# Kernel optimization log

Hardware: AMD Instinct MI355X
Metric: run time of the kernel (lower is better)

Reference implementation:

```python
import jax, jax.numpy as jnp
import numpy as np
import math

N = 10000; E = 160000; B = 16
H = 256; TD = 128; NB = 4; NL = 3; NAT = 100; CD = 3


def _silu(x):
    return x * jax.nn.sigmoid(x)


def _mlp2(x, w1, b1, w2, b2):
    return _silu(x @ w1 + b1) @ w2 + b2


def _ln(x, g, b):
    m = jnp.mean(x, -1, keepdims=True)
    v = jnp.mean((x - m) ** 2, -1, keepdims=True)
    return (x - m) / jnp.sqrt(v + 1e-5) * g + b


def _fwd(x_atoms, pos, edge_index, batch_idx, timesteps, conditions, emb,
         te_w1, te_b1, te_w2, te_b2, ce_w1, ce_b1, ce_w2, ce_b2,
         tp_w1, tp_b1, tp_w2, tp_b2, nm_w1, nm_b1, nm_w2, nm_b2,
         em_w1, em_b1, em_w2, em_b2, ln_g, ln_b,
         ao_w1, ao_b1, ao_w2, ao_b2, co_w1, co_b1, co_w2, co_b2):
    n = x_atoms.shape[0]
    row, col = edge_index[0], edge_index[1]  # row = source (x_j), col = target (x_i)
    h = emb[x_atoms]  # [N, H]
    half = TD // 2
    freqs = jnp.exp(jnp.arange(half, dtype=jnp.float32) * (-math.log(10000.0) / (half - 1)))
    ang = timesteps.astype(jnp.float32)[:, None] * freqs[None, :]
    time_emb = _mlp2(jnp.concatenate([jnp.sin(ang), jnp.cos(ang)], -1), te_w1, te_b1, te_w2, te_b2)
    time_emb = time_emb + _mlp2(conditions, ce_w1, ce_b1, ce_w2, ce_b2)  # [B, TD]
    rel = pos[row] - pos[col]
    dist = jnp.sqrt(jnp.sum(rel * rel, -1, keepdims=True))  # [E, 1]
    counts = jnp.maximum(
        jax.ops.segment_sum(jnp.ones((row.shape[0],), jnp.float32), col, num_segments=n), 1.0)[:, None]
    for b in range(NB):
        h = h + _mlp2(time_emb, tp_w1[b], tp_b1[b], tp_w2[b], tp_b2[b])[batch_idx]
        for l in range(NL):
            # message: edge_mlp(concat(x_i, x_j, dist)); PyG x_i = target = col, x_j = source = row
            msg = _mlp2(jnp.concatenate([h[col], h[row], dist], -1),
                        em_w1[b, l], em_b1[b, l], em_w2[b, l], em_b2[b, l])  # [E, H]
            agg = jax.ops.segment_sum(msg, col, num_segments=n) / counts  # mean aggregation
            h_new = _mlp2(h, nm_w1[b, l], nm_b1[b, l], nm_w2[b, l], nm_b2[b, l]) + agg
            h = _ln(h + h_new, ln_g[b, l], ln_b[b, l])
    atom = _mlp2(h, ao_w1, ao_b1, ao_w2, ao_b2)  # [N, NAT]
    coord = _mlp2(h, co_w1, co_b1, co_w2, co_b2)  # [N, 3]
    return atom, coord


def setup_inputs() -> dict:
    key = jax.random.key(0)
    ks = jax.random.split(key, 48)
    ki = iter(ks)

    def nrm(shape, s=0.02):
        return jax.random.normal(next(ki), shape, jnp.float32) * s

    x_atoms = jax.random.randint(next(ki), (N,), 0, NAT)
    pos = jax.random.normal(next(ki), (N, 3), jnp.float32)
    row = jax.random.randint(next(ki), (E,), 0, N)
    off = jax.random.randint(next(ki), (E,), 1, N)
    col = (row + off) % N  # avoid self-loops so dist > 0
    edge_index = jnp.stack([row, col])
    batch_idx = jnp.sort(jax.random.randint(next(ki), (N,), 0, B))
    timesteps = jax.random.randint(next(ki), (B,), 0, 1000)
    conditions = jax.random.normal(next(ki), (B, CD), jnp.float32)
    z = lambda s: jnp.zeros(s, jnp.float32)
    params = dict(
        emb=nrm((NAT, H)),
        te_w1=nrm((TD, 2 * TD)), te_b1=z((2 * TD,)), te_w2=nrm((2 * TD, TD)), te_b2=z((TD,)),
        ce_w1=nrm((CD, H)), ce_b1=z((H,)), ce_w2=nrm((H, TD)), ce_b2=z((TD,)),
        tp_w1=nrm((NB, TD, H)), tp_b1=z((NB, H)), tp_w2=nrm((NB, H, H)), tp_b2=z((NB, H)),
        nm_w1=nrm((NB, NL, H, H)), nm_b1=z((NB, NL, H)), nm_w2=nrm((NB, NL, H, H)), nm_b2=z((NB, NL, H)),
        em_w1=nrm((NB, NL, 2 * H + 1, H)), em_b1=z((NB, NL, H)), em_w2=nrm((NB, NL, H, H)), em_b2=z((NB, NL, H)),
        ln_g=jnp.ones((NB, NL, H), jnp.float32), ln_b=z((NB, NL, H)),
        ao_w1=nrm((H, H)), ao_b1=z((H,)), ao_w2=nrm((H, NAT)), ao_b2=z((NAT,)),
        co_w1=nrm((H, H)), co_b1=z((H,)), co_w2=nrm((H, 3)), co_b2=z((3,)),
    )
    return dict(x_atoms=x_atoms, pos=pos, edge_index=edge_index, batch_idx=batch_idx,
                timesteps=timesteps, conditions=conditions, **params)


def reference(x_atoms, pos, edge_index, batch_idx, timesteps, conditions, emb,
              te_w1, te_b1, te_w2, te_b2, ce_w1, ce_b1, ce_w2, ce_b2,
              tp_w1, tp_b1, tp_w2, tp_b2, nm_w1, nm_b1, nm_w2, nm_b2,
              em_w1, em_b1, em_w2, em_b2, ln_g, ln_b,
              ao_w1, ao_b1, ao_w2, ao_b2, co_w1, co_b1, co_w2, co_b2):
    return _fwd(x_atoms, pos, edge_index, batch_idx, timesteps, conditions, emb,
                te_w1, te_b1, te_w2, te_b2, ce_w1, ce_b1, ce_w2, ce_b2,
                tp_w1, tp_b1, tp_w2, tp_b2, nm_w1, nm_b1, nm_w2, nm_b2,
                em_w1, em_b1, em_w2, em_b2, ln_g, ln_b,
                ao_w1, ao_b1, ao_w2, ao_b2, co_w1, co_b1, co_w2, co_b2)
```

## Files before the change

### kernel.cpp

```cpp
#include <hip/hip_runtime.h>

typedef unsigned short u16;
typedef __attribute__((ext_vector_type(8))) short   bf16x8;
typedef __attribute__((ext_vector_type(4))) float   f32x4;
typedef __attribute__((ext_vector_type(4))) unsigned short u16x4;
typedef __attribute__((ext_vector_type(2))) unsigned short u16x2;

#define DEV __device__ __forceinline__

DEV float bf2f(u16 u){ return __uint_as_float(((unsigned)u)<<16); }
DEV u16 f2bf(float f){ unsigned x=__float_as_uint(f); unsigned r=x+0x7fffu+((x>>16)&1u); return (u16)(r>>16); }
DEV float silu_f(float x){
  float e = __expf(-x);
  return x * __builtin_amdgcn_rcpf(1.f + e);
}
DEV float ldf(const void* p, long i, int isbf){
  float r;
  if (isbf) r = bf2f(((const u16*)p)[i]);
  else      r = ((const float*)p)[i];
  return r;
}
template<int ISBF> DEV float LD(const void* p, long i){
  if (ISBF) return bf2f(((const u16*)p)[i]);
  return ((const float*)p)[i];
}

#define GLDS(g,l) __builtin_amdgcn_global_load_lds((const __attribute__((address_space(1))) void*)(g), (__attribute__((address_space(3))) void*)(l), 16, 0, 0)

__global__ void k_detect(const unsigned* __restrict__ lng, int* __restrict__ flag){
  if (threadIdx.x == 0 && blockIdx.x == 0)
    flag[0] = (lng[0] == 0x3F800000u) ? 0 : 1;
}

__global__ __launch_bounds__(256) void k_packparams(
    const void* nm_b1, const void* em_b1, const void* nm_b2, const void* em_b2,
    const void* ln_g, const void* ln_b, const void* em_w1,
    const void* ao_b1, const void* co_b1, const void* ao_b2,
    const void* co_w2, const void* co_b2,
    const int* __restrict__ flagp, float* __restrict__ pp){
  int isbf = flagp[0];
  int i = blockIdx.x*256 + threadIdx.x;
  if (i >= 22887) return;
  const int T1 = 3072;
  float v;
  if      (i < T1)    v = ldf(nm_b1, i, isbf);
  else if (i < 2*T1)  v = ldf(em_b1, i-T1, isbf);
  else if (i < 3*T1)  v = ldf(nm_b2, i-2*T1, isbf);
  else if (i < 4*T1)  v = ldf(em_b2, i-3*T1, isbf);
  else if (i < 5*T1)  v = ldf(ln_g, i-4*T1, isbf);
  else if (i < 6*T1)  v = ldf(ln_b, i-5*T1, isbf);
  else if (i < 7*T1){ int j=i-6*T1; int li=j>>8; v = ldf(em_w1, (long)li*513*256 + 512*256 + (j&255), isbf); }
  else if (i < 22016){ int j=i-21504; v = (j<256) ? ldf(ao_b1,j,isbf) : ldf(co_b1,j-256,isbf); }
  else if (i < 22116) v = ldf(ao_b2, i-22016, isbf);
  else if (i < 22884) v = ldf(co_w2, i-22116, isbf);
  else                v = ldf(co_b2, i-22884, isbf);
  pp[i] = v;
}

template<int ISBF>
DEV void wtpose_body(const void* in, long inoff, long ims, int istride, int Ncin,
                     u16* out, long obase, int ors, long oms){
  __shared__ float tile[64][65];
  int k0 = blockIdx.x*64, j0 = blockIdx.y*64;
  long m = blockIdx.z;
  int t = threadIdx.x;
  int c = t & 63, r4 = t >> 6;
  #pragma unroll
  for (int pass=0; pass<16; pass++){
    int k = k0 + pass*4 + r4;
    int j = j0 + c;
    float v = 0.f;
    if (j < Ncin) v = LD<ISBF>(in, inoff + m*ims + (long)k*istride + j);
    tile[pass*4 + r4][c] = v;
  }
  __syncthreads();
  #pragma unroll
  for (int pass=0; pass<16; pass++){
    int j = j0 + pass*4 + r4;
    int k = k0 + c;
    out[m*oms + obase + (long)j*ors + k] = f2bf(tile[c][pass*4 + r4]);
  }
}
__global__ __launch_bounds__(256) void k_wtpose(const void* in, long inoff, long ims, int istride, int Ncin,
                        u16* out, long obase, int ors, long oms, const int* __restrict__ flagp){
  if (flagp[0]) wtpose_body<1>(in, inoff, ims, istride, Ncin, out, obase, ors, oms);
  else          wtpose_body<0>(in, inoff, ims, istride, Ncin, out, obase, ors, oms);
}

template<int ISBF>
DEV void timeembed_body(const int* tsteps, const void* cond,
    const void* te_w1, const void* te_b1, const void* te_w2, const void* te_b2,
    const void* ce_w1, const void* ce_b1, const void* ce_w2, const void* ce_b2,
    float* time_emb){
  __shared__ float sa[256], sb[256];
  int b = blockIdx.x, t = threadIdx.x;
  float ts = (float)tsteps[b];
  if (t < 64){
    float coef = (float)(-9.210340371976184/63.0);
    float fr = __expf(coef * (float)t);
    float ang = ts * fr;
    sa[t]      = sinf(ang);
    sa[64 + t] = cosf(ang);
  }
  __syncthreads();
  {
    float a = LD<ISBF>(te_b1, t);
    float s0=0.f,s1=0.f,s2=0.f,s3=0.f;
    #pragma unroll
    for (int k=0;k<128;k+=4){
      s0 += sa[k  ]*LD<ISBF>(te_w1,(k  )*256+t);
      s1 += sa[k+1]*LD<ISBF>(te_w1,(k+1)*256+t);
      s2 += sa[k+2]*LD<ISBF>(te_w1,(k+2)*256+t);
      s3 += sa[k+3]*LD<ISBF>(te_w1,(k+3)*256+t);
    }
    sb[t] = silu_f(a + ((s0+s1)+(s2+s3)));
  }
  __syncthreads();
  float te = 0.f;
  if (t < 128){
    float s0=0.f,s1=0.f,s2=0.f,s3=0.f;
    #pragma unroll
    for (int k=0;k<256;k+=4){
      s0 += sb[k  ]*LD<ISBF>(te_w2,(k  )*128+t);
      s1 += sb[k+1]*LD<ISBF>(te_w2,(k+1)*128+t);
      s2 += sb[k+2]*LD<ISBF>(te_w2,(k+2)*128+t);
      s3 += sb[k+3]*LD<ISBF>(te_w2,(k+3)*128+t);
    }
    te = LD<ISBF>(te_b2, t) + ((s0+s1)+(s2+s3));
  }
  {
    float a = LD<ISBF>(ce_b1, t);
    #pragma unroll
    for (int k=0;k<3;k++) a += LD<ISBF>(cond, b*3 + k)*LD<ISBF>(ce_w1, k*256 + t);
    float v = silu_f(a);
    __syncthreads();
    sa[t] = v;
  }
  __syncthreads();
  if (t < 128){
    float s0=0.f,s1=0.f,s2=0.f,s3=0.f;
    #pragma unroll
    for (int k=0;k<256;k+=4){
      s0 += sa[k  ]*LD<ISBF>(ce_w2,(k  )*128+t);
      s1 += sa[k+1]*LD<ISBF>(ce_w2,(k+1)*128+t);
      s2 += sa[k+2]*LD<ISBF>(ce_w2,(k+2)*128+t);
      s3 += sa[k+3]*LD<ISBF>(ce_w2,(k+3)*128+t);
    }
    float ce = LD<ISBF>(ce_b2, t) + ((s0+s1)+(s2+s3));
    time_emb[b*128 + t] = te + ce;
  }
}
__global__ __launch_bounds__(256) void k_timeembed(
    const int* tsteps, const void* cond,
    const void* te_w1, const void* te_b1, const void* te_w2, const void* te_b2,
    const void* ce_w1, const void* ce_b1, const void* ce_w2, const void* ce_b2,
    const int* __restrict__ flagp, float* time_emb){
  if (flagp[0]) timeembed_body<1>(tsteps,cond,te_w1,te_b1,te_w2,te_b2,ce_w1,ce_b1,ce_w2,ce_b2,time_emb);
  else          timeembed_body<0>(tsteps,cond,te_w1,te_b1,te_w2,te_b2,ce_w1,ce_b1,ce_w2,ce_b2,time_emb);
}

template<int ISBF>
DEV void timeproj_body(const float* time_emb, const void* tp_w1, const void* tp_b1,
                       const void* tp_w2, const void* tp_b2, float* tpe){
  __shared__ float x[128];
  __shared__ float tm[256];
  int b4 = blockIdx.x >> 4, b = blockIdx.x & 15, t = threadIdx.x;
  if (t < 128) x[t] = time_emb[b*128 + t];
  __syncthreads();
  {
    float s0=0.f,s1=0.f,s2=0.f,s3=0.f;
    #pragma unroll
    for (int k=0;k<128;k+=4){
      s0 += x[k  ]*LD<ISBF>(tp_w1, ((long)b4*128 + k  )*256 + t);
      s1 += x[k+1]*LD<ISBF>(tp_w1, ((long)b4*128 + k+1)*256 + t);
      s2 += x[k+2]*LD<ISBF>(tp_w1, ((long)b4*128 + k+2)*256 + t);
      s3 += x[k+3]*LD<ISBF>(tp_w1, ((long)b4*128 + k+3)*256 + t);
    }
    float a = LD<ISBF>(tp_b1, b4*256 + t) + ((s0+s1)+(s2+s3));
    tm[t] = silu_f(a);
  }
  __syncthreads();
  float s0=0.f,s1=0.f,s2=0.f,s3=0.f;
  #pragma unroll
  for (int k=0;k<256;k+=4){
    s0 += tm[k  ]*LD<ISBF>(tp_w2, ((long)b4*256 + k  )*256 + t);
    s1 += tm[k+1]*LD<ISBF>(tp_w2, ((long)b4*256 + k+1)*256 + t);
    s2 += tm[k+2]*LD<ISBF>(tp_w2, ((long)b4*256 + k+2)*256 + t);
    s3 += tm[k+3]*LD<ISBF>(tp_w2, ((long)b4*256 + k+3)*256 + t);
  }
  float o = LD<ISBF>(tp_b2, b4*256 + t) + ((s0+s1)+(s2+s3));
  tpe[((long)b4*16 + b)*256 + t] = o;
}
__global__ __launch_bounds__(256) void k_timeproj(
    const float* time_emb, const void* tp_w1, const void* tp_b1,
    const void* tp_w2, const void* tp_b2, const int* __restrict__ flagp, float* tpe){
  if (flagp[0]) timeproj_body<1>(time_emb, tp_w1, tp_b1, tp_w2, tp_b2, tpe);
  else          timeproj_body<0>(time_emb, tp_w1, tp_b1, tp_w2, tp_b2, tpe);
}

template<int ISBF>
DEV void edgegeo_body(const int* ei, const void* pos, float* dist, int* cnt, int E){
  int e = blockIdx.x*256 + threadIdx.x;
  if (e >= E) return;
  int r = ei[e], c = ei[E + e];
  float dx = LD<ISBF>(pos,(long)r*3+0) - LD<ISBF>(pos,(long)c*3+0);
  float dy = LD<ISBF>(pos,(long)r*3+1) - LD<ISBF>(pos,(long)c*3+1);
  float dz = LD<ISBF>(pos,(long)r*3+2) - LD<ISBF>(pos,(long)c*3+2);
  dist[e] = sqrtf(dx*dx + dy*dy + dz*dz);
  atomicAdd(&cnt[c], 1);
}
__global__ __launch_bounds__(256) void k_edgegeo(const int* ei, const void* pos,
                          const int* __restrict__ flagp, float* dist, int* cnt, int E){
  if (flagp[0]) edgegeo_body<1>(ei,pos,dist,cnt,E);
  else          edgegeo_body<0>(ei,pos,dist,cnt,E);
}

__global__ __launch_bounds__(1024) void k_scan(const int* __restrict__ cnt, int* __restrict__ basep, int n){
  __shared__ int s[1024];
  int t = threadIdx.x;
  int running = 0;
  int nch = (n + 1023) >> 10;
  for (int ch=0; ch<nch; ch++){
    int i = ch*1024 + t;
    int v = (i < n) ? cnt[i] : 0;
    s[t] = v;
    __syncthreads();
    for (int off=1; off<1024; off<<=1){
      int add = (t >= off) ? s[t-off] : 0;
      __syncthreads();
      s[t] += add;
      __syncthreads();
    }
    if (i < n) basep[i] = running + s[t] - v;
    running += s[1023];
    __syncthreads();
  }
  if (t == 0) basep[n] = running;
}

__global__ __launch_bounds__(256) void k_scatter(const int* __restrict__ ei, const int* __restrict__ basep,
                          int* __restrict__ cursor, int* __restrict__ perm, int E){
  int e = blockIdx.x*256 + threadIdx.x;
  if (e >= E) return;
  int c = ei[E + e];
  int p = atomicAdd(&cursor[c], 1);
  perm[basep[c] + p] = e;
}

template<int ISBF>
DEV void embed_body(const int* xa, const void* emb, const float* tpe0, const int* bidx,
                    float* h, u16* hb, int total){
  int idx = blockIdx.x*256 + threadIdx.x;
  if (idx >= total) return;
  int row = idx >> 8, col = idx & 255;
  float v = LD<ISBF>(emb, (long)xa[row]*256 + col) + tpe0[bidx[row]*256 + col];
  h[idx] = v;
  hb[idx] = f2bf(v);
}
__global__ __launch_bounds__(256) void k_embed(const int* xa, const void* emb,
                        const int* __restrict__ flagp, const float* tpe0, const int* bidx,
                        float* h, u16* hb, int total){
  if (flagp[0]) embed_body<1>(xa, emb, tpe0, bidx, h, hb, total);
  else          embed_body<0>(xa, emb, tpe0, bidx, h, hb, total);
}

__global__ __launch_bounds__(256) void k_agg(
    const u16* __restrict__ PQ, const int* __restrict__ perm, const int* __restrict__ basep,
    const int* __restrict__ rows, const float* __restrict__ dist,
    const float* __restrict__ w1rf, const float* __restrict__ b1f,
    const int* __restrict__ cnt, u16* __restrict__ A2, int n){
  int w = threadIdx.x >> 6, lane = threadIdx.x & 63;
  int node = blockIdx.x*2 + (w >> 1);
  if (node >= n) return;
  int half = w & 1;
  int c0 = half*128 + lane*2;
  u16x2 pv = *(const u16x2*)&PQ[(long)node*512 + c0];
  float pb0 = bf2f(pv[0]) + b1f[c0];
  float pb1 = bf2f(pv[1]) + b1f[c0+1];
  float wr0 = w1rf[c0], wr1 = w1rf[c0+1];
  float acc0 = 0.f, acc1 = 0.f;
  int s = basep[node], e = basep[node+1];
  const u16* Qb = PQ + 256 + c0;
  for (int q0=s; q0<e; q0+=64){
    int m = e - q0; if (m > 64) m = 64;
    int   rl = 0; float dl = 0.f;
    if (lane < m){ int ed = perm[q0+lane]; rl = rows[ed]; dl = dist[ed]; }
    int q = 0;
    for (; q+4<=m; q+=4){
      int   r0 = __shfl(rl, q,   64), r1 = __shfl(rl, q+1, 64);
      int   r2 = __shfl(rl, q+2, 64), r3 = __shfl(rl, q+3, 64);
      float d0 = __shfl(dl, q,   64), d1 = __shfl(dl, q+1, 64);
      float d2 = __shfl(dl, q+2, 64), d3 = __shfl(dl, q+3, 64);
      u16x2 qv0 = *(const u16x2*)&Qb[(long)r0*512];
      u16x2 qv1 = *(const u16x2*)&Qb[(long)r1*512];
      u16x2 qv2 = *(const u16x2*)&Qb[(long)r2*512];
      u16x2 qv3 = *(const u16x2*)&Qb[(long)r3*512];
      acc0 += silu_f(fmaf(d0, wr0, pb0 + bf2f(qv0[0])));
      acc1 += silu_f(fmaf(d0, wr1, pb1 + bf2f(qv0[1])));
      acc0 += silu_f(fmaf(d1, wr0, pb0 + bf2f(qv1[0])));
      acc1 += silu_f(fmaf(d1, wr1, pb1 + bf2f(qv1[1])));
      acc0 += silu_f(fmaf(d2, wr0, pb0 + bf2f(qv2[0])));
      acc1 += silu_f(fmaf(d2, wr1, pb1 + bf2f(qv2[1])));
      acc0 += silu_f(fmaf(d3, wr0, pb0 + bf2f(qv3[0])));
      acc1 += silu_f(fmaf(d3, wr1, pb1 + bf2f(qv3[1])));
    }
    for (; q<m; q++){
      int   r = __shfl(rl, q, 64);
      float d = __shfl(dl, q, 64);
      u16x2 qv = *(const u16x2*)&Qb[(long)r*512];
      acc0 += silu_f(fmaf(d, wr0, pb0 + bf2f(qv[0])));
      acc1 += silu_f(fmaf(d, wr1, pb1 + bf2f(qv[1])));
    }
  }
  int cc = cnt[node];
  float inv = __builtin_amdgcn_rcpf((float)(cc > 0 ? cc : 1));
  u16x2 o; o[0] = f2bf(acc0*inv); o[1] = f2bf(acc1*inv);
  *(u16x2*)&A2[(long)node*512 + 256 + c0] = o;
}

__global__ __launch_bounds__(256) void k_co2(
    const u16* __restrict__ UV, const float* __restrict__ w, const float* __restrict__ b,
    const int* __restrict__ flagp, void* __restrict__ out, long n100, int n){
  int isbf = flagp[0];
  int row = blockIdx.x*4 + (threadIdx.x >> 6);
  if (row >= n) return;
  int lane = threadIdx.x & 63;
  int k0 = lane*4;
  u16x4 vv = *(const u16x4*)&UV[(long)row*512 + 256 + k0];
  float a0=0.f, a1=0.f, a2=0.f;
  #pragma unroll
  for (int j=0;j<4;j++){
    float v = bf2f(vv[j]);
    a0 += v*w[(k0+j)*3+0];
    a1 += v*w[(k0+j)*3+1];
    a2 += v*w[(k0+j)*3+2];
  }
  #pragma unroll
  for (int o=32;o>=1;o>>=1){ a0 += __shfl_xor(a0,o,64); a1 += __shfl_xor(a1,o,64); a2 += __shfl_xor(a2,o,64); }
  if (lane == 0){
    float r0 = a0 + b[0], r1 = a1 + b[1], r2 = a2 + b[2];
    if (isbf){
      u16* o = (u16*)out + n100 + (long)row*3;
      o[0] = f2bf(r0); o[1] = f2bf(r1); o[2] = f2bf(r2);
    } else {
      float* o = (float*)out + n100 + (long)row*3;
      o[0] = r0; o[1] = r1; o[2] = r2;
    }
  }
}

template<int TM, int MODE>
__global__ __launch_bounds__(256) void k_gemm(
    const u16* __restrict__ A, int lda, const u16* __restrict__ Wt,
    void* __restrict__ D0, void* __restrict__ D1,
    const float* __restrict__ bf1,
    const int* __restrict__ flagp, int M, int K, int nbn){
  constexpr int MR = TM/32;
  __shared__ __align__(16) u16 As[TM*64];
  __shared__ __align__(16) u16 Bs[128*64];
  const int bid = blockIdx.x;
  const int mb = bid / nbn, nb = bid - mb*nbn;
  const int bm0 = mb*TM, bn0 = nb*128;
  const int t = threadIdx.x;
  const int w = t >> 6, lane = t & 63;
  const int wr = w >> 1, wc = w & 1;
  const int swz8 = ((lane & 7) ^ (lane >> 3)) * 8;

  f32x4 acc[MR][4];
  #pragma unroll
  for (int m=0;m<MR;m++)
    #pragma unroll
    for (int n=0;n<4;n++){ f32x4 z = {0.f,0.f,0.f,0.f}; acc[m][n] = z; }

  long baseA[TM/32];
  #pragma unroll
  for (int i=0;i<TM/32;i++){
    int r = bm0 + i*32 + w*8 + (lane>>3);
    if (r > M-1) r = M-1;
    baseA[i] = (long)r*lda + swz8;
  }
  long baseB[4];
  #pragma unroll
  for (int i=0;i<4;i++){
    int r = bn0 + i*32 + w*8 + (lane>>3);
    baseB[i] = (long)r*K + swz8;
  }

  const int rA = lane & 15;
  const int sx = rA & 7;
  const int qhi = lane >> 4;

  for (int kt=0; kt<K; kt+=64){
    #pragma unroll
    for (int i=0;i<TM/32;i++) GLDS(A  + baseA[i] + kt, As + (i*32 + w*8)*64);
    #pragma unroll
    for (int i=0;i<4;i++)     GLDS(Wt + baseB[i] + kt, Bs + (i*32 + w*8)*64);
    __syncthreads();
    #pragma unroll
    for (int kk=0;kk<2;kk++){
      const int punit = ((kk*4 + qhi) ^ sx) * 8;
      bf16x8 af[MR], bv[4];
      #pragma unroll
      for (int m=0;m<MR;m++)
        af[m] = *(const bf16x8*)&As[(wr*(TM/2) + m*16 + rA)*64 + punit];
      #pragma unroll
      for (int n=0;n<4;n++)
        bv[n] = *(const bf16x8*)&Bs[(wc*64 + n*16 + rA)*64 + punit];
      #pragma unroll
      for (int m=0;m<MR;m++)
        #pragma unroll
        for (int n=0;n<4;n++)
          acc[m][n] = __builtin_amdgcn_mfma_f32_16x16x32_bf16(af[m], bv[n], acc[m][n], 0, 0, 0);
    }
    __syncthreads();
  }

  const int rg = lane >> 4, cix = lane & 15;
  const int isbf = (MODE==3) ? flagp[0] : 0;
  #pragma unroll
  for (int n=0;n<4;n++){
    const int col = bn0 + wc*64 + n*16 + cix;
    float b1v = 0.f;
    if (MODE==0){ if (col>=512) b1v = bf1[col-512]; }
    else if (MODE==2){ b1v = bf1[col]; }
    else { if (col<100) b1v = bf1[col]; }
    #pragma unroll
    for (int m=0;m<MR;m++){
      const int rbase = bm0 + wr*(TM/2) + m*16 + rg*4;
      #pragma unroll
      for (int r=0;r<4;r++){
        const int row = rbase + r;
        if (row >= M) continue;
        float v = acc[m][n][r];
        if (MODE==0){
          if (col < 512) ((u16*)D0)[(long)row*512 + col] = f2bf(v);
          else           ((u16*)D1)[(long)row*512 + (col-512)] = f2bf(silu_f(v + b1v));
        } else if (MODE==2){
          ((u16*)D0)[(long)row*512 + col] = f2bf(silu_f(v + b1v));
        } else {
          if (col < 100){
            v += b1v;
            if (isbf) ((u16*)D0)[(long)row*100 + col] = f2bf(v);
            else      ((float*)D0)[(long)row*100 + col] = v;
          }
        }
      }
    }
  }
}

__global__ __launch_bounds__(256) void k_gemmln(
    const u16* __restrict__ A, const u16* __restrict__ Wt,
    float* __restrict__ h, u16* __restrict__ hb,
    const float* __restrict__ b1f, const float* __restrict__ b2f,
    const float* __restrict__ gf, const float* __restrict__ bbf,
    const int* __restrict__ cnt,
    const float* __restrict__ tpe, const int* __restrict__ bidx,
    int M, int K){
  __shared__ __align__(16) u16 As[32*64];
  __shared__ __align__(16) u16 Bs[256*64];
  const int bm0 = blockIdx.x*32;
  const int t = threadIdx.x;
  const int w = t >> 6, lane = t & 63;
  const int wc = w;
  const int swz8 = ((lane & 7) ^ (lane >> 3)) * 8;

  f32x4 acc[2][4];
  #pragma unroll
  for (int m=0;m<2;m++)
    #pragma unroll
    for (int n=0;n<4;n++){ f32x4 z = {0.f,0.f,0.f,0.f}; acc[m][n] = z; }

  long baseA;
  { int r = bm0 + w*8 + (lane>>3); if (r > M-1) r = M-1; baseA = (long)r*512 + swz8; }
  long baseB[8];
  #pragma unroll
  for (int i=0;i<8;i++){
    int r = i*32 + w*8 + (lane>>3);
    baseB[i] = (long)r*K + swz8;
  }

  const int rA = lane & 15;
  const int sx = rA & 7;
  const int qhi = lane >> 4;

  for (int kt=0; kt<K; kt+=64){
    GLDS(A + baseA + kt, As + (w*8)*64);
    #pragma unroll
    for (int i=0;i<8;i++) GLDS(Wt + baseB[i] + kt, Bs + (i*32 + w*8)*64);
    __syncthreads();
    #pragma unroll
    for (int kk=0;kk<2;kk++){
      const int punit = ((kk*4 + qhi) ^ sx) * 8;
      bf16x8 af[2], bv[4];
      #pragma unroll
      for (int m=0;m<2;m++)
        af[m] = *(const bf16x8*)&As[(m*16 + rA)*64 + punit];
      #pragma unroll
      for (int n=0;n<4;n++)
        bv[n] = *(const bf16x8*)&Bs[(wc*64 + n*16 + rA)*64 + punit];
      #pragma unroll
      for (int m=0;m<2;m++)
        #pragma unroll
        for (int n=0;n<4;n++)
          acc[m][n] = __builtin_amdgcn_mfma_f32_16x16x32_bf16(af[m], bv[n], acc[m][n], 0, 0, 0);
    }
    __syncthreads();
  }

  const int rg = lane >> 4, cix = lane & 15;
  float ps[2][4], pq[2][4];
  #pragma unroll
  for (int m=0;m<2;m++){
    #pragma unroll
    for (int r=0;r<4;r++){
      const int row = bm0 + m*16 + rg*4 + r;
      const int rowc = (row < M) ? row : (M-1);
      const float hmask = (cnt[rowc] > 0) ? 1.f : 0.f;
      float s = 0.f, q = 0.f;
      #pragma unroll
      for (int n=0;n<4;n++){
        const int col = wc*64 + n*16 + cix;
        float v = acc[m][n][r] + b1f[col] + hmask*b2f[col] + h[(long)rowc*256 + col];
        acc[m][n][r] = v;
        s += v; q += v*v;
      }
      ps[m][r] = s; pq[m][r] = q;
    }
  }
  #pragma unroll
  for (int m=0;m<2;m++)
    #pragma unroll
    for (int r=0;r<4;r++){
      #pragma unroll
      for (int o=8;o>=1;o>>=1){
        ps[m][r] += __shfl_xor(ps[m][r], o, 64);
        pq[m][r] += __shfl_xor(pq[m][r], o, 64);
      }
    }
  float* sred = (float*)As;
  if (cix == 0){
    #pragma unroll
    for (int m=0;m<2;m++)
      #pragma unroll
      for (int r=0;r<4;r++){
        int rl = m*16 + rg*4 + r;
        sred[w*32 + rl]       = ps[m][r];
        sred[128 + w*32 + rl] = pq[m][r];
      }
  }
  __syncthreads();
  #pragma unroll
  for (int m=0;m<2;m++){
    #pragma unroll
    for (int r=0;r<4;r++){
      const int rl = m*16 + rg*4 + r;
      const int row = bm0 + rl;
      if (row >= M) continue;
      float S = sred[rl] + sred[32+rl] + sred[64+rl] + sred[96+rl];
      float Q = sred[128+rl] + sred[160+rl] + sred[192+rl] + sred[224+rl];
      float mean = S * (1.f/256.f);
      float var  = Q * (1.f/256.f) - mean*mean;
      float rs = rsqrtf(var + 1e-5f);
      const float* tb = tpe ? (tpe + (long)bidx[row]*256) : nullptr;
      #pragma unroll
      for (int n=0;n<4;n++){
        const int col = wc*64 + n*16 + cix;
        float y = (acc[m][n][r]-mean)*rs*gf[col] + bbf[col];
        if (tb) y += tb[col];
        h[(long)row*256 + col] = y;
        hb[(long)row*256 + col] = f2bf(y);
      }
    }
  }
}

extern "C" void kernel_launch(void* const* d_in, const int* in_sizes, int n_in,
                              void* d_out, int out_size, void* d_ws, size_t ws_size,
                              hipStream_t stream)
{
  const int N  = in_sizes[0];
  const int E  = in_sizes[2] / 2;
  const int H  = 256;
  const int MB128 = (N + 127)/128;
  const int MB64  = (N + 63)/64;
  const int MB32  = (N + 31)/32;

  const int*  x_atoms = (const int*)d_in[0];
  const void* pos     = d_in[1];
  const int*  ei      = (const int*)d_in[2];
  const int*  bidx    = (const int*)d_in[3];
  const int*  tsteps  = (const int*)d_in[4];
  const void* cond    = d_in[5];
  const void* emb     = d_in[6];
  const void* te_w1   = d_in[7];
  const void* te_b1   = d_in[8];
  const void* te_w2   = d_in[9];
  const void* te_b2   = d_in[10];
  const void* ce_w1   = d_in[11];
  const void* ce_b1   = d_in[12];
  const void* ce_w2   = d_in[13];
  const void* ce_b2   = d_in[14];
  const void* tp_w1   = d_in[15];
  const void* tp_b1   = d_in[16];
  const void* tp_w2   = d_in[17];
  const void* tp_b2   = d_in[18];
  const void* nm_w1   = d_in[19];
  const void* nm_b1   = d_in[20];
  const void* nm_w2   = d_in[21];
  const void* nm_b2   = d_in[22];
  const void* em_w1   = d_in[23];
  const void* em_b1   = d_in[24];
  const void* em_w2   = d_in[25];
  const void* em_b2   = d_in[26];
  const void* ln_g    = d_in[27];
  const void* ln_b    = d_in[28];
  const void* ao_w1   = d_in[29];
  const void* ao_b1   = d_in[30];
  const void* ao_w2   = d_in[31];
  const void* ao_b2   = d_in[32];
  const void* co_w1   = d_in[33];
  const void* co_b1   = d_in[34];
  const void* co_w2   = d_in[35];
  const void* co_b2   = d_in[36];

  char* wp = (char*)d_ws;
  auto alloc = [&](size_t bytes)->char*{ char* p = wp; wp += (bytes + 255) & ~(size_t)255; return p; };
  int*   flagp   = (int*)  alloc(256);
  float* h_f32   = (float*)alloc((size_t)N*H*4);
  u16*   hb16    = (u16*)  alloc((size_t)N*H*2);
  u16*   PQ      = (u16*)  alloc((size_t)N*512*2);
  u16*   A2      = (u16*)  alloc((size_t)N*512*2);
  u16*   UV      = PQ;
  float* dist    = (float*)alloc((size_t)E*4);
  int*   perm    = (int*)  alloc((size_t)E*4);
  int*   basep   = (int*)  alloc((size_t)(N+1)*4);
  int*   cnt     = (int*)  alloc((size_t)N*4);
  int*   cursor  = (int*)  alloc((size_t)N*4);
  float* time_emb= (float*)alloc((size_t)16*128*4);
  float* tpe     = (float*)alloc((size_t)4*16*256*4);
  u16*   pqtW    = (u16*)  alloc((size_t)12*768*256*2);
  u16*   w2stk   = (u16*)  alloc((size_t)12*256*512*2);
  u16*   UVw     = (u16*)  alloc((size_t)512*256*2);
  u16*   ao_w2t  = (u16*)  alloc((size_t)128*256*2);
  float* pp      = (float*)alloc((size_t)22887*4);

  const float* nm_b1f = pp;
  const float* em_b1f = pp + 3072;
  const float* nm_b2f = pp + 6144;
  const float* em_b2f = pp + 9216;
  const float* ln_gf  = pp + 12288;
  const float* ln_bf  = pp + 15360;
  const float* w1rf   = pp + 18432;
  const float* headbf = pp + 21504;
  const float* ao_b2f = pp + 22016;
  const float* co_w2f = pp + 22116;
  const float* co_b2f = pp + 22884;

  hipMemsetAsync(cnt,    0, (size_t)N*4, stream);
  hipMemsetAsync(cursor, 0, (size_t)N*4, stream);

  k_detect<<<1, 1, 0, stream>>>((const unsigned*)ln_g, flagp);
  k_packparams<<<(22887+255)/256, 256, 0, stream>>>(nm_b1, em_b1, nm_b2, em_b2, ln_g, ln_b, em_w1,
                                                    ao_b1, co_b1, ao_b2, co_w2, co_b2, flagp, pp);

  auto WT = [&](const void* in, long inoff, long ims, int istride, int Ncin,
                u16* out, long obase, int ors, long oms, int J, int nmat){
    k_wtpose<<<dim3(4, J/64, nmat), 256, 0, stream>>>(in, inoff, ims, istride, Ncin,
                                                      out, obase, ors, oms, flagp);
  };
  WT(em_w1, 0,        513*256, 256, 256, pqtW, 0,        256, 768*256, 256, 12);
  WT(em_w1, 256*256,  513*256, 256, 256, pqtW, 256*256,  256, 768*256, 256, 12);
  WT(nm_w1, 0,        256*256, 256, 256, pqtW, 512*256,  256, 768*256, 256, 12);
  WT(nm_w2, 0,        256*256, 256, 256, w2stk, 0,       512, 256*512, 256, 12);
  WT(em_w2, 0,        256*256, 256, 256, w2stk, 256,     512, 256*512, 256, 12);
  WT(ao_w1, 0,        0,       256, 256, UVw,  0,        256, 0,       256, 1);
  WT(co_w1, 0,        0,       256, 256, UVw,  256*256,  256, 0,       256, 1);
  WT(ao_w2, 0,        0,       100, 100, ao_w2t, 0,      256, 0,       128, 1);

  k_timeembed<<<16, 256, 0, stream>>>(tsteps, cond, te_w1, te_b1, te_w2, te_b2,
                                      ce_w1, ce_b1, ce_w2, ce_b2, flagp, time_emb);
  k_timeproj<<<64, 256, 0, stream>>>(time_emb, tp_w1, tp_b1, tp_w2, tp_b2, flagp, tpe);

  k_edgegeo<<<(E+255)/256, 256, 0, stream>>>(ei, pos, flagp, dist, cnt, E);
  k_scan<<<1, 1024, 0, stream>>>(cnt, basep, N);
  k_scatter<<<(E+255)/256, 256, 0, stream>>>(ei, basep, cursor, perm, E);

  k_embed<<<(N*H+255)/256, 256, 0, stream>>>(x_atoms, emb, flagp, tpe, bidx, h_f32, hb16, N*H);

  for (int b4 = 0; b4 < 4; b4++){
    for (int l = 0; l < 3; l++){
      int li = b4*3 + l;
      k_gemm<128,0><<<MB128*6, 256, 0, stream>>>(hb16, 256, pqtW + (long)li*768*256,
                                                 PQ, A2, nm_b1f + li*256,
                                                 flagp, N, 256, 6);
      k_agg<<<(N+1)/2, 256, 0, stream>>>(PQ, perm, basep, ei, dist,
                                         w1rf + li*256, em_b1f + li*256, cnt, A2, N);
      const float* tpe_next = (l == 2 && b4 < 3) ? (tpe + (long)(b4+1)*16*256) : nullptr;
      k_gemmln<<<MB32, 256, 0, stream>>>(A2, w2stk + (long)li*256*512,
                                         h_f32, hb16,
                                         nm_b2f + li*256, em_b2f + li*256,
                                         ln_gf + li*256, ln_bf + li*256,
                                         cnt, tpe_next, bidx, N, 512);
    }
  }

  k_gemm<128,2><<<MB128*4, 256, 0, stream>>>(hb16, 256, UVw, UV, nullptr, headbf,
                                             flagp, N, 256, 4);
  k_gemm<64,3><<<MB64*1, 256, 0, stream>>>(UV, 512, ao_w2t, d_out, nullptr, ao_b2f,
                                           flagp, N, 256, 1);
  k_co2<<<(N+3)/4, 256, 0, stream>>>(UV, co_w2f, co_b2f, flagp, d_out, (long)N*100, N);
}
```

Before: 889.8 us.

## Merge setup kernels, fuse time MLPs, use wave-shuffle scan, swizzle GEMM blocks across XCDs

Folds dtype detection into the parameter-pack kernel and merges the eight weight-transpose launches into one job-table kernel. Fuses the time-embedding and time-projection MLPs into a single kernel that stages weight chunks in LDS. Replaces the barrier-heavy Hillis-Steele block scan with a wavefront shuffle scan. Remaps GEMM block IDs across XCDs for better L2 locality. Together these cut launch count and setup overhead. In exchange the fused time kernel recomputes the time embedding 4x per batch element, once for each of the four projection blocks.

```diff
diff --git a/kernel.cpp b/kernel.cpp
--- a/kernel.cpp
+++ b/kernel.cpp
@@ -27,9 +27,10 @@
 
 #define GLDS(g,l) __builtin_amdgcn_global_load_lds((const __attribute__((address_space(1))) void*)(g), (__attribute__((address_space(3))) void*)(l), 16, 0, 0)
 
-__global__ void k_detect(const unsigned* __restrict__ lng, int* __restrict__ flag){
-  if (threadIdx.x == 0 && blockIdx.x == 0)
-    flag[0] = (lng[0] == 0x3F800000u) ? 0 : 1;
+DEV int xcd_swz(int bid, int nwg){
+  int q = nwg >> 3, r = nwg & 7;
+  int x = bid & 7, l = bid >> 3;
+  return (x < r ? x*(q+1) : r*(q+1) + (x-r)*q) + l;
 }
 
 __global__ __launch_bounds__(256) void k_packparams(
@@ -37,9 +38,10 @@
     const void* ln_g, const void* ln_b, const void* em_w1,
     const void* ao_b1, const void* co_b1, const void* ao_b2,
     const void* co_w2, const void* co_b2,
-    const int* __restrict__ flagp, float* __restrict__ pp){
-  int isbf = flagp[0];
+    int* __restrict__ flagp, float* __restrict__ pp){
+  int isbf = (((const unsigned*)ln_g)[0] == 0x3F800000u) ? 0 : 1;
   int i = blockIdx.x*256 + threadIdx.x;
+  if (i == 0) flagp[0] = isbf;
   if (i >= 22887) return;
   const int T1 = 3072;
   float v;
@@ -57,12 +59,25 @@
   pp[i] = v;
 }
 
+struct WTJob {
+  const void* in; long inoff; long ims; long obase; long oms;
+  u16* out; int istride; int Ncin; int ors; int gx; int gy;
+};
+struct WTJobs { WTJob j[8]; int tile0[8]; };
+
 template<int ISBF>
-DEV void wtpose_body(const void* in, long inoff, long ims, int istride, int Ncin,
-                     u16* out, long obase, int ors, long oms){
+DEV void wtall_body(const WTJobs& J){
+  int bidx = blockIdx.x;
+  int ji = 0;
+  #pragma unroll
+  for (int j=1;j<8;j++) if (bidx >= J.tile0[j]) ji = j;
+  const WTJob& job = J.j[ji];
+  int ti = bidx - J.tile0[ji];
+  int kx = ti % job.gx;
+  int jy = (ti / job.gx) % job.gy;
+  long m  = ti / (job.gx * job.gy);
+  int k0 = kx*64, j0 = jy*64;
   __shared__ float tile[64][65];
-  int k0 = blockIdx.x*64, j0 = blockIdx.y*64;
-  long m = blockIdx.z;
   int t = threadIdx.x;
   int c = t & 63, r4 = t >> 6;
   #pragma unroll
@@ -70,7 +85,7 @@
     int k = k0 + pass*4 + r4;
     int j = j0 + c;
     float v = 0.f;
-    if (j < Ncin) v = LD<ISBF>(in, inoff + m*ims + (long)k*istride + j);
+    if (j < job.Ncin) v = LD<ISBF>(job.in, job.inoff + m*job.ims + (long)k*job.istride + j);
     tile[pass*4 + r4][c] = v;
   }
   __syncthreads();
@@ -78,22 +93,23 @@
   for (int pass=0; pass<16; pass++){
     int j = j0 + pass*4 + r4;
     int k = k0 + c;
-    out[m*oms + obase + (long)j*ors + k] = f2bf(tile[c][pass*4 + r4]);
-  }
-}
-__global__ __launch_bounds__(256) void k_wtpose(const void* in, long inoff, long ims, int istride, int Ncin,
-                        u16* out, long obase, int ors, long oms, const int* __restrict__ flagp){
-  if (flagp[0]) wtpose_body<1>(in, inoff, ims, istride, Ncin, out, obase, ors, oms);
-  else          wtpose_body<0>(in, inoff, ims, istride, Ncin, out, obase, ors, oms);
+    job.out[m*job.oms + job.obase + (long)j*job.ors + k] = f2bf(tile[c][pass*4 + r4]);
+  }
+}
+__global__ __launch_bounds__(256) void k_wtall(WTJobs J, const int* __restrict__ flagp){
+  if (flagp[0]) wtall_body<1>(J);
+  else          wtall_body<0>(J);
 }
 
 template<int ISBF>
-DEV void timeembed_body(const int* tsteps, const void* cond,
+DEV void time_body(const int* tsteps, const void* cond,
     const void* te_w1, const void* te_b1, const void* te_w2, const void* te_b2,
     const void* ce_w1, const void* ce_b1, const void* ce_w2, const void* ce_b2,
-    float* time_emb){
-  __shared__ float sa[256], sb[256];
-  int b = blockIdx.x, t = threadIdx.x;
+    const void* tp_w1, const void* tp_b1, const void* tp_w2, const void* tp_b2,
+    float* tpe){
+  __shared__ float wbuf[8192];
+  __shared__ float sa[256], sb[256], tm[256], tb[128];
+  int b4 = blockIdx.x >> 4, b = blockIdx.x & 15, t = threadIdx.x;
   float ts = (float)tsteps[b];
   if (t < 64){
     float coef = (float)(-9.210340371976184/63.0);
@@ -103,99 +119,67 @@
     sa[64 + t] = cosf(ang);
   }
   __syncthreads();
-  {
-    float a = LD<ISBF>(te_b1, t);
-    float s0=0.f,s1=0.f,s2=0.f,s3=0.f;
-    #pragma unroll
-    for (int k=0;k<128;k+=4){
-      s0 += sa[k  ]*LD<ISBF>(te_w1,(k  )*256+t);
-      s1 += sa[k+1]*LD<ISBF>(te_w1,(k+1)*256+t);
-      s2 += sa[k+2]*LD<ISBF>(te_w1,(k+2)*256+t);
-      s3 += sa[k+3]*LD<ISBF>(te_w1,(k+3)*256+t);
-    }
-    sb[t] = silu_f(a + ((s0+s1)+(s2+s3)));
-  }
-  __syncthreads();
-  float te = 0.f;
-  if (t < 128){
-    float s0=0.f,s1=0.f,s2=0.f,s3=0.f;
-    #pragma unroll
-    for (int k=0;k<256;k+=4){
-      s0 += sb[k  ]*LD<ISBF>(te_w2,(k  )*128+t);
-      s1 += sb[k+1]*LD<ISBF>(te_w2,(k+1)*128+t);
-      s2 += sb[k+2]*LD<ISBF>(te_w2,(k+2)*128+t);
-      s3 += sb[k+3]*LD<ISBF>(te_w2,(k+3)*128+t);
-    }
-    te = LD<ISBF>(te_b2, t) + ((s0+s1)+(s2+s3));
-  }
-  {
-    float a = LD<ISBF>(ce_b1, t);
-    #pragma unroll
-    for (int k=0;k<3;k++) a += LD<ISBF>(cond, b*3 + k)*LD<ISBF>(ce_w1, k*256 + t);
-    float v = silu_f(a);
-    __syncthreads();
-    sa[t] = v;
-  }
-  __syncthreads();
-  if (t < 128){
-    float s0=0.f,s1=0.f,s2=0.f,s3=0.f;
-    #pragma unroll
-    for (int k=0;k<256;k+=4){
-      s0 += sa[k  ]*LD<ISBF>(ce_w2,(k  )*128+t);
-      s1 += sa[k+1]*LD<ISBF>(ce_w2,(k+1)*128+t);
-      s2 += sa[k+2]*LD<ISBF>(ce_w2,(k+2)*128+t);
-      s3 += sa[k+3]*LD<ISBF>(ce_w2,(k+3)*128+t);
-    }
-    float ce = LD<ISBF>(ce_b2, t) + ((s0+s1)+(s2+s3));
-    time_emb[b*128 + t] = te + ce;
-  }
-}
-__global__ __launch_bounds__(256) void k_timeembed(
+  float a1 = LD<ISBF>(te_b1, t);
+  for (int ck=0; ck<128; ck+=32){
+    for (int i=t;i<8192;i+=256) wbuf[i] = LD<ISBF>(te_w1, (long)ck*256 + i);
+    __syncthreads();
+    #pragma unroll 8
+    for (int k=0;k<32;k++) a1 += sa[ck+k]*wbuf[k*256+t];
+    __syncthreads();
+  }
+  sb[t] = silu_f(a1);
+  float te = (t<128) ? LD<ISBF>(te_b2, t) : 0.f;
+  for (int ck=0; ck<256; ck+=64){
+    for (int i=t;i<8192;i+=256) wbuf[i] = LD<ISBF>(te_w2, (long)ck*128 + i);
+    __syncthreads();
+    if (t<128){
+      #pragma unroll 8
+      for (int k=0;k<64;k++) te += sb[ck+k]*wbuf[k*128+t];
+    }
+    __syncthreads();
+  }
+  float a2 = LD<ISBF>(ce_b1, t);
+  #pragma unroll
+  for (int k=0;k<3;k++) a2 += LD<ISBF>(cond, b*3+k)*LD<ISBF>(ce_w1, k*256+t);
+  sa[t] = silu_f(a2);
+  float ce = (t<128) ? LD<ISBF>(ce_b2, t) : 0.f;
+  for (int ck=0; ck<256; ck+=64){
+    for (int i=t;i<8192;i+=256) wbuf[i] = LD<ISBF>(ce_w2, (long)ck*128 + i);
+    __syncthreads();
+    if (t<128){
+      #pragma unroll 8
+      for (int k=0;k<64;k++) ce += sa[ck+k]*wbuf[k*128+t];
+    }
+    __syncthreads();
+  }
+  if (t<128) tb[t] = te + ce;
+  float a3 = LD<ISBF>(tp_b1, b4*256 + t);
+  for (int ck=0; ck<128; ck+=32){
+    for (int i=t;i<8192;i+=256) wbuf[i] = LD<ISBF>(tp_w1, ((long)b4*128+ck)*256 + i);
+    __syncthreads();
+    #pragma unroll 8
+    for (int k=0;k<32;k++) a3 += tb[ck+k]*wbuf[k*256+t];
+    __syncthreads();
+  }
+  tm[t] = silu_f(a3);
+  float a4 = LD<ISBF>(tp_b2, b4*256 + t);
+  for (int ck=0; ck<256; ck+=32){
+    for (int i=t;i<8192;i+=256) wbuf[i] = LD<ISBF>(tp_w2, ((long)b4*256+ck)*256 + i);
+    __syncthreads();
+    #pragma unroll 8
+    for (int k=0;k<32;k++) a4 += tm[ck+k]*wbuf[k*256+t];
+    __syncthreads();
+  }
+  tpe[((long)b4*16 + b)*256 + t] = a4;
+}
+__global__ __launch_bounds__(256) void k_time(
     const int* tsteps, const void* cond,
     const void* te_w1, const void* te_b1, const void* te_w2, const void* te_b2,
     const void* ce_w1, const void* ce_b1, const void* ce_w2, const void* ce_b2,
-    const int* __restrict__ flagp, float* time_emb){
-  if (flagp[0]) timeembed_body<1>(tsteps,cond,te_w1,te_b1,te_w2,te_b2,ce_w1,ce_b1,ce_w2,ce_b2,time_emb);
-  else          timeembed_body<0>(tsteps,cond,te_w1,te_b1,te_w2,te_b2,ce_w1,ce_b1,ce_w2,ce_b2,time_emb);
-}
-
-template<int ISBF>
-DEV void timeproj_body(const float* time_emb, const void* tp_w1, const void* tp_b1,
-                       const void* tp_w2, const void* tp_b2, float* tpe){
-  __shared__ float x[128];
-  __shared__ float tm[256];
-  int b4 = blockIdx.x >> 4, b = blockIdx.x & 15, t = threadIdx.x;
-  if (t < 128) x[t] = time_emb[b*128 + t];
-  __syncthreads();
-  {
-    float s0=0.f,s1=0.f,s2=0.f,s3=0.f;
-    #pragma unroll
-    for (int k=0;k<128;k+=4){
-      s0 += x[k  ]*LD<ISBF>(tp_w1, ((long)b4*128 + k  )*256 + t);
-      s1 += x[k+1]*LD<ISBF>(tp_w1, ((long)b4*128 + k+1)*256 + t);
-      s2 += x[k+2]*LD<ISBF>(tp_w1, ((long)b4*128 + k+2)*256 + t);
-      s3 += x[k+3]*LD<ISBF>(tp_w1, ((long)b4*128 + k+3)*256 + t);
-    }
-    float a = LD<ISBF>(tp_b1, b4*256 + t) + ((s0+s1)+(s2+s3));
-    tm[t] = silu_f(a);
-  }
-  __syncthreads();
-  float s0=0.f,s1=0.f,s2=0.f,s3=0.f;
-  #pragma unroll
-  for (int k=0;k<256;k+=4){
-    s0 += tm[k  ]*LD<ISBF>(tp_w2, ((long)b4*256 + k  )*256 + t);
-    s1 += tm[k+1]*LD<ISBF>(tp_w2, ((long)b4*256 + k+1)*256 + t);
-    s2 += tm[k+2]*LD<ISBF>(tp_w2, ((long)b4*256 + k+2)*256 + t);
-    s3 += tm[k+3]*LD<ISBF>(tp_w2, ((long)b4*256 + k+3)*256 + t);
-  }
-  float o = LD<ISBF>(tp_b2, b4*256 + t) + ((s0+s1)+(s2+s3));
-  tpe[((long)b4*16 + b)*256 + t] = o;
-}
-__global__ __launch_bounds__(256) void k_timeproj(
-    const float* time_emb, const void* tp_w1, const void* tp_b1,
-    const void* tp_w2, const void* tp_b2, const int* __restrict__ flagp, float* tpe){
-  if (flagp[0]) timeproj_body<1>(time_emb, tp_w1, tp_b1, tp_w2, tp_b2, tpe);
-  else          timeproj_body<0>(time_emb, tp_w1, tp_b1, tp_w2, tp_b2, tpe);
+    const void* tp_w1, const void* tp_b1, const void* tp_w2, const void* tp_b2,
+    const int* __restrict__ flagp, float* tpe){
+  if (flagp[0]) time_body<1>(tsteps,cond,te_w1,te_b1,te_w2,te_b2,ce_w1,ce_b1,ce_w2,ce_b2,tp_w1,tp_b1,tp_w2,tp_b2,tpe);
+  else          time_body<0>(tsteps,cond,te_w1,te_b1,te_w2,te_b2,ce_w1,ce_b1,ce_w2,ce_b2,tp_w1,tp_b1,tp_w2,tp_b2,tpe);
 }
 
 template<int ISBF>
@@ -216,23 +200,26 @@
 }
 
 __global__ __launch_bounds__(1024) void k_scan(const int* __restrict__ cnt, int* __restrict__ basep, int n){
-  __shared__ int s[1024];
-  int t = threadIdx.x;
+  __shared__ int wsum[16];
+  int t = threadIdx.x, w = t >> 6, lane = t & 63;
   int running = 0;
   int nch = (n + 1023) >> 10;
   for (int ch=0; ch<nch; ch++){
     int i = ch*1024 + t;
     int v = (i < n) ? cnt[i] : 0;
-    s[t] = v;
-    __syncthreads();
-    for (int off=1; off<1024; off<<=1){
-      int add = (t >= off) ? s[t-off] : 0;
-      __syncthreads();
-      s[t] += add;
-      __syncthreads();
-    }
-    if (i < n) basep[i] = running + s[t] - v;
-    running += s[1023];
+    int sc = v;
+    #pragma unroll
+    for (int off=1; off<64; off<<=1){
+      int u = __shfl_up(sc, off, 64);
+      if (lane >= off) sc += u;
+    }
+    if (lane == 63) wsum[w] = sc;
+    __syncthreads();
+    int wexcl = 0, tot = 0;
+    #pragma unroll
+    for (int j=0;j<16;j++){ int x = wsum[j]; if (j < w) wexcl += x; tot += x; }
+    if (i < n) basep[i] = running + wexcl + sc - v;
+    running += tot;
     __syncthreads();
   }
   if (t == 0) basep[n] = running;
@@ -358,7 +345,7 @@
   constexpr int MR = TM/32;
   __shared__ __align__(16) u16 As[TM*64];
   __shared__ __align__(16) u16 Bs[128*64];
-  const int bid = blockIdx.x;
+  const int bid = xcd_swz(blockIdx.x, gridDim.x);
   const int mb = bid / nbn, nb = bid - mb*nbn;
   const int bm0 = mb*TM, bn0 = nb*128;
   const int t = threadIdx.x;
@@ -637,7 +624,6 @@
   int*   basep   = (int*)  alloc((size_t)(N+1)*4);
   int*   cnt     = (int*)  alloc((size_t)N*4);
   int*   cursor  = (int*)  alloc((size_t)N*4);
-  float* time_emb= (float*)alloc((size_t)16*128*4);
   float* tpe     = (float*)alloc((size_t)4*16*256*4);
   u16*   pqtW    = (u16*)  alloc((size_t)12*768*256*2);
   u16*   w2stk   = (u16*)  alloc((size_t)12*256*512*2);
@@ -660,27 +646,31 @@
   hipMemsetAsync(cnt,    0, (size_t)N*4, stream);
   hipMemsetAsync(cursor, 0, (size_t)N*4, stream);
 
-  k_detect<<<1, 1, 0, stream>>>((const unsigned*)ln_g, flagp);
   k_packparams<<<(22887+255)/256, 256, 0, stream>>>(nm_b1, em_b1, nm_b2, em_b2, ln_g, ln_b, em_w1,
                                                     ao_b1, co_b1, ao_b2, co_w2, co_b2, flagp, pp);
 
-  auto WT = [&](const void* in, long inoff, long ims, int istride, int Ncin,
-                u16* out, long obase, int ors, long oms, int J, int nmat){
-    k_wtpose<<<dim3(4, J/64, nmat), 256, 0, stream>>>(in, inoff, ims, istride, Ncin,
-                                                      out, obase, ors, oms, flagp);
+  WTJobs J;
+  auto setjob = [&](int idx, const void* in, long inoff, long ims, int istride, int Ncin,
+                    u16* out, long obase, int ors, long oms, int gx, int gy, int gz){
+    J.j[idx] = WTJob{ in, inoff, ims, obase, oms, out, istride, Ncin, ors, gx, gy };
+    J.tile0[idx] = (idx == 0) ? 0 : 0;
+    return gx*gy*gz;
   };
-  WT(em_w1, 0,        513*256, 256, 256, pqtW, 0,        256, 768*256, 256, 12);
-  WT(em_w1, 256*256,  513*256, 256, 256, pqtW, 256*256,  256, 768*256, 256, 12);
-  WT(nm_w1, 0,        256*256, 256, 256, pqtW, 512*256,  256, 768*256, 256, 12);
-  WT(nm_w2, 0,        256*256, 256, 256, w2stk, 0,       512, 256*512, 256, 12);
-  WT(em_w2, 0,        256*256, 256, 256, w2stk, 256,     512, 256*512, 256, 12);
-  WT(ao_w1, 0,        0,       256, 256, UVw,  0,        256, 0,       256, 1);
-  WT(co_w1, 0,        0,       256, 256, UVw,  256*256,  256, 0,       256, 1);
-  WT(ao_w2, 0,        0,       100, 100, ao_w2t, 0,      256, 0,       128, 1);
-
-  k_timeembed<<<16, 256, 0, stream>>>(tsteps, cond, te_w1, te_b1, te_w2, te_b2,
-                                      ce_w1, ce_b1, ce_w2, ce_b2, flagp, time_emb);
-  k_timeproj<<<64, 256, 0, stream>>>(time_emb, tp_w1, tp_b1, tp_w2, tp_b2, flagp, tpe);
+  int tacc = 0;
+  int tn;
+  tn = setjob(0, em_w1, 0,        513*256, 256, 256, pqtW,  0,        256, 768*256, 4, 4, 12); J.tile0[0]=tacc; tacc+=tn;
+  tn = setjob(1, em_w1, 256*256,  513*256, 256, 256, pqtW,  256*256,  256, 768*256, 4, 4, 12); J.tile0[1]=tacc; tacc+=tn;
+  tn = setjob(2, nm_w1, 0,        256*256, 256, 256, pqtW,  512*256,  256, 768*256, 4, 4, 12); J.tile0[2]=tacc; tacc+=tn;
+  tn = setjob(3, nm_w2, 0,        256*256, 256, 256, w2stk, 0,        512, 256*512, 4, 4, 12); J.tile0[3]=tacc; tacc+=tn;
+  tn = setjob(4, em_w2, 0,        256*256, 256, 256, w2stk, 256,      512, 256*512, 4, 4, 12); J.tile0[4]=tacc; tacc+=tn;
+  tn = setjob(5, ao_w1, 0,        0,       256, 256, UVw,   0,        256, 0,       4, 4, 1);  J.tile0[5]=tacc; tacc+=tn;
+  tn = setjob(6, co_w1, 0,        0,       256, 256, UVw,   256*256,  256, 0,       4, 4, 1);  J.tile0[6]=tacc; tacc+=tn;
+  tn = setjob(7, ao_w2, 0,        0,       100, 100, ao_w2t,0,        256, 0,       4, 2, 1);  J.tile0[7]=tacc; tacc+=tn;
+  k_wtall<<<tacc, 256, 0, stream>>>(J, flagp);
+
+  k_time<<<64, 256, 0, stream>>>(tsteps, cond, te_w1, te_b1, te_w2, te_b2,
+                                 ce_w1, ce_b1, ce_w2, ce_b2,
+                                 tp_w1, tp_b1, tp_w2, tp_b2, flagp, tpe);
 
   k_edgegeo<<<(E+255)/256, 256, 0, stream>>>(ei, pos, flagp, dist, cnt, E);
   k_scan<<<1, 1024, 0, stream>>>(cnt, basep, N);
```

Measured after the change: 875.2 us. No clear change (-1.6%).
